# Optimization experiments

Hardware: AMD Instinct MI355X
Metric: run time of the kernel (lower is better)

## Reference

```python
import jax, jax.numpy as jnp
import numpy as np
import math

D_MODEL = 128
N_HEADS = 8
D_FF = 512
FACTOR = 3
EPS = 1e-5


def _ln(x, g, b):
    mu = x.mean(-1, keepdims=True)
    var = ((x - mu) ** 2).mean(-1, keepdims=True)
    return (x - mu) / jnp.sqrt(var + EPS) * g + b


def setup_inputs() -> dict:
    key = jax.random.key(0)
    ks = jax.random.split(key, 16)
    d, dff = D_MODEL, D_FF
    s = 0.02
    return {
        "x": jax.random.normal(ks[0], (4, 32, 256), dtype=jnp.float32),
        "mlp_w": jax.random.normal(ks[1], (d,)) * s,  # Conv2d(1,d,1x1) weight squeezed
        "mlp_b": jnp.zeros((d,), jnp.float32),
        "wq": jax.random.normal(ks[2], (d, d)) * s, "bq": jnp.zeros((d,), jnp.float32),
        "wk": jax.random.normal(ks[3], (d, d)) * s, "bk": jnp.zeros((d,), jnp.float32),
        "wv": jax.random.normal(ks[4], (d, d)) * s, "bv": jnp.zeros((d,), jnp.float32),
        "wo": jax.random.normal(ks[5], (d, d)) * s, "bo": jnp.zeros((d,), jnp.float32),
        "w1": jax.random.normal(ks[6], (dff, d)) * s, "b1": jnp.zeros((dff,), jnp.float32),
        "w2": jax.random.normal(ks[7], (d, dff)) * s, "b2": jnp.zeros((d,), jnp.float32),
        "ln1_g": jnp.ones((d,), jnp.float32), "ln1_b": jnp.zeros((d,), jnp.float32),
        "ln2_g": jnp.ones((d,), jnp.float32), "ln2_b": jnp.zeros((d,), jnp.float32),
    }


def reference(x, mlp_w, mlp_b, wq, bq, wk, bk, wv, bv, wo, bo,
              w1, b1, w2, b2, ln1_g, ln1_b, ln2_g, ln2_b):
    b, N, T = x.shape
    C, H = D_MODEL, N_HEADS
    E = C // H
    # 1x1 Conv2d from 1 channel -> per-channel affine of scalar input
    h = x[..., None] * mlp_w + mlp_b                      # [b,N,T,C]
    h = h.reshape(b * N, T, C)                            # [B,L,C]
    B, L = h.shape[0], T
    q = (h @ wq.T + bq).reshape(B, L, H, E).transpose(0, 2, 1, 3)  # [B,H,L,E]
    k = (h @ wk.T + bk).reshape(B, L, H, E).transpose(0, 2, 1, 3)
    v = (h @ wv.T + bv).reshape(B, L, H, E).transpose(0, 2, 1, 3)

    sample_k = min(FACTOR * math.ceil(math.log(L)), L)
    u = min(FACTOR * math.ceil(math.log(L)), L)
    # random K-sample indices shared across batch/heads (torch.randint analogue)
    idx = jax.random.randint(jax.random.key(42), (L, sample_k), 0, L)

    scores_full = jnp.einsum('bhle,bhse->bhls', q, k)     # [B,H,L,L]
    qk_sample = jnp.take_along_axis(scores_full, idx[None, None], axis=-1)  # [B,H,L,sample_k]
    M = qk_sample.max(-1) - qk_sample.sum(-1) / L         # sparsity measure
    m_top = jax.lax.top_k(M, u)[1]                        # [B,H,u] top-u query indices
    scores_top = jnp.take_along_axis(scores_full, m_top[..., None], axis=2)  # [B,H,u,L]
    scores_top = scores_top / math.sqrt(E)

    attn = jax.nn.softmax(scores_top, axis=-1)
    upd = jnp.einsum('bhul,bhle->bhue', attn, v)          # [B,H,u,E]
    # mask_flag=False: initial context = mean(V) broadcast over queries
    context = jnp.broadcast_to(v.mean(axis=2, keepdims=True), v.shape)
    bi = jnp.arange(B)[:, None, None]
    hi = jnp.arange(H)[None, :, None]
    context = context.at[bi, hi, m_top].set(upd)          # scatter top-u updates

    out = context.transpose(0, 2, 1, 3).reshape(B, L, C) @ wo.T + bo
    x1 = _ln(h + out, ln1_g, ln1_b)
    y = jax.nn.relu(x1 @ w1.T + b1) @ w2.T + b2           # 1x1 conv1d pair == MLP
    out2 = _ln(x1 + y, ln2_g, ln2_b)
    out2 = out2.reshape(b, N, T, C).sum(axis=1)           # sum over N
    return out2.transpose(0, 2, 1)                        # [b,C,T]
```

## Files before the change

kernel.cpp:

```cpp
#include <hip/hip_runtime.h>
#include <stdint.h>
#include <math.h>


#define EPSF 1e-5f

typedef short bf16x8 __attribute__((ext_vector_type(8)));
typedef float f32x4  __attribute__((ext_vector_type(4)));

__device__ __forceinline__ unsigned short f2bf(float f) {
  union { float f; unsigned u; } v; v.f = f;
  unsigned r = v.u + 0x7FFFu + ((v.u >> 16) & 1u);
  return (unsigned short)(r >> 16);
}
__device__ __forceinline__ float bf2f(unsigned short u) {
  union { unsigned u; float f; } v; v.u = ((unsigned)u) << 16;
  return v.f;
}
__device__ __forceinline__ float waveSum(float v) {
  #pragma unroll
  for (int m = 32; m > 0; m >>= 1) v += __shfl_xor(v, m);
  return v;
}

__device__ __forceinline__ void threefry2x32_k42(uint32_t& x0, uint32_t& x1) {
  const uint32_t ks0 = 0u, ks1 = 42u, ks2 = 0u ^ 42u ^ 0x1BD11BDAu;
  x0 += ks0; x1 += ks1;
#define TF_R(d) { x0 += x1; x1 = (x1 << d) | (x1 >> (32 - d)); x1 ^= x0; }
  TF_R(13) TF_R(15) TF_R(26) TF_R(6)  x0 += ks1; x1 += ks2 + 1u;
  TF_R(17) TF_R(29) TF_R(16) TF_R(24) x0 += ks2; x1 += ks0 + 2u;
  TF_R(13) TF_R(15) TF_R(26) TF_R(6)  x0 += ks0; x1 += ks1 + 3u;
  TF_R(17) TF_R(29) TF_R(16) TF_R(24) x0 += ks1; x1 += ks2 + 4u;
  TF_R(13) TF_R(15) TF_R(26) TF_R(6)  x0 += ks2; x1 += ks0 + 5u;
#undef TF_R
}

__global__ __launch_bounds__(256) void setup_kernel(
    const float* __restrict__ mlp_w, const float* __restrict__ mlp_b,
    const float* __restrict__ wq, const float* __restrict__ bq,
    const float* __restrict__ wk, const float* __restrict__ bk,
    const float* __restrict__ wv, const float* __restrict__ bv,
    const float* __restrict__ wo, const float* __restrict__ bo,
    const float* __restrict__ w1, const float* __restrict__ w2,
    int* __restrict__ idxT, float* __restrict__ cst,
    unsigned short* __restrict__ w1s, unsigned short* __restrict__ w2s) {
  int tid = threadIdx.x;
  {
    int fid = blockIdx.x * 256 + tid;
    const float* s;
    unsigned short* d;
    if (fid < 8192) {
      int lane = fid & 63; int tmp = fid >> 6;
      int ft = tmp & 3; tmp >>= 2;
      int ks = tmp & 3; tmp >>= 2;
      int ch = tmp & 1; int w = tmp >> 1;
      int col = lane & 15, quad = lane >> 4;
      int f = w * 128 + ch * 64 + ft * 16 + col;
      int k = ks * 32 + quad * 8;
      s = w1 + f * 128 + k;
      d = w1s + fid * 8;
    } else {
      int G = fid - 8192;
      int lane = G & 63; int tmp = G >> 6;
      int tc = tmp & 7; tmp >>= 3;
      int kk = tmp & 1; tmp >>= 1;
      int ch = tmp & 1; int w = tmp >> 1;
      int col = lane & 15, quad = lane >> 4;
      int c = tc * 16 + col;
      int k = w * 128 + ch * 64 + kk * 32 + quad * 8;
      s = w2 + c * 512 + k;
      d = w2s + G * 8;
    }
    float4 v0 = *(const float4*)s, v1 = *(const float4*)(s + 4);
    uint4 pk;
    pk.x = (unsigned)f2bf(v0.x) | ((unsigned)f2bf(v0.y) << 16);
    pk.y = (unsigned)f2bf(v0.z) | ((unsigned)f2bf(v0.w) << 16);
    pk.z = (unsigned)f2bf(v1.x) | ((unsigned)f2bf(v1.y) << 16);
    pk.w = (unsigned)f2bf(v1.z) | ((unsigned)f2bf(v1.w) << 16);
    *(uint4*)d = pk;
  }
  if (blockIdx.x != 0) return;
  for (int p = tid; p < 2304; p += 256) {
    uint32_t a = (uint32_t)p, bb = (uint32_t)(p + 2304);
    threefry2x32_k42(a, bb);
    int l0 = p / 18, j0 = p - l0 * 18;
    int p2 = p + 2304;
    int l1 = p2 / 18, j1 = p2 - l1 * 18;
    idxT[j0 * 256 + l0] = (int)(a & 0xFFu);
    idxT[j1 * 256 + l1] = (int)(bb & 0xFFu);
  }
  if (tid < 128) {
    float aq = 0.f, cq_ = 0.f, ak = 0.f, ck_ = 0.f, av = 0.f, cv_ = 0.f;
    for (int c = 0; c < 128; c++) {
      float w = mlp_w[c], bb = mlp_b[c];
      float q = wq[tid * 128 + c], k = wk[tid * 128 + c], v = wv[tid * 128 + c];
      aq += q * w; cq_ += q * bb;
      ak += k * w; ck_ += k * bb;
      av += v * w; cv_ += v * bb;
    }
    cst[0   + tid] = aq;
    cst[128 + tid] = cq_ + bq[tid];
    cst[256 + tid] = ak;
    cst[384 + tid] = ck_ + bk[tid];
    cst[512 + tid] = av;
    cst[640 + tid] = cv_ + bv[tid];
  }
  __syncthreads();
  if (tid < 8) {
    float a = 0.f, b = 0.f, g = 0.f, d = 0.f;
    for (int e = 0; e < 16; e++) {
      int j = tid * 16 + e;
      float Aq = cst[j], Cq = cst[128 + j], Ak = cst[256 + j], Ck = cst[384 + j];
      a += Aq * Ak; b += Aq * Ck; g += Cq * Ak; d += Cq * Ck;
    }
    cst[768 + tid] = a; cst[776 + tid] = b; cst[784 + tid] = g; cst[792 + tid] = d;
  }
  if (tid < 128) {
    float oc = 0.f;
    for (int h = 0; h < 8; h++) {
      float s = 0.f;
      for (int e = 0; e < 16; e++) {
        float w = wo[tid * 128 + h * 16 + e];
        s  += w * cst[512 + h * 16 + e];
        oc += w * cst[640 + h * 16 + e];
      }
      cst[800 + h * 128 + tid] = s;
    }
    cst[1824 + tid] = oc + bo[tid] + mlp_b[tid];
  }
}

__global__ __launch_bounds__(256) void attn_kernel(
    const float* __restrict__ x, const int* __restrict__ idxT,
    const float* __restrict__ cst, float* __restrict__ g) {
  __shared__ float xr[256];
  __shared__ float Mb[512];
  __shared__ float selv[512];
  __shared__ float rsum[4], rmax[4], rmin[4];
  __shared__ int   items[64];
  __shared__ float witem[64];
  __shared__ int   cnt;
  int tid = threadIdx.x, lane = tid & 63, w = tid >> 6;
  int seq = blockIdx.x >> 2, hg = blockIdx.x & 3;
  if (tid == 0) cnt = 0;
  float xv = x[seq * 256 + tid];
  xr[tid] = xv;
  float s = waveSum(xv);
  float mx = xv, mn = xv;
  #pragma unroll
  for (int m = 32; m > 0; m >>= 1) {
    mx = fmaxf(mx, __shfl_xor(mx, m));
    mn = fminf(mn, __shfl_xor(mn, m));
  }
  if (lane == 0) { rsum[w] = s; rmax[w] = mx; rmin[w] = mn; }
  __syncthreads();
  float meanx = (rsum[0] + rsum[1] + rsum[2] + rsum[3]) * (1.0f / 256.0f);
  float maxx = fmaxf(fmaxf(rmax[0], rmax[1]), fmaxf(rmax[2], rmax[3]));
  float minx = fminf(fminf(rmin[0], rmin[1]), fminf(rmin[2], rmin[3]));
  int l32 = tid & 31, grp = tid >> 5;
  float xs8[8];
  #pragma unroll
  for (int k = 0; k < 8; k++) xs8[k] = xr[l32 + k * 32];
  float mx18 = -INFINITY, mn18 = INFINITY, s18 = 0.f;
  #pragma unroll 3
  for (int j = 0; j < 18; j++) {
    float xs = xr[idxT[j * 256 + tid]];
    mx18 = fmaxf(mx18, xs); mn18 = fminf(mn18, xs); s18 += xs;
  }
  int h0 = hg * 2, h1 = h0 + 1;
  float al0 = cst[768 + h0], be0 = cst[776 + h0], ga0 = cst[784 + h0], de0 = cst[792 + h0];
  float al1 = cst[768 + h1], be1 = cst[776 + h1], ga1 = cst[784 + h1], de1 = cst[792 + h1];
  float ac0 = fmaf(al0, xv, ga0), cc0 = fmaf(be0, xv, de0);
  float ac1 = fmaf(al1, xv, ga1), cc1 = fmaf(be1, xv, de1);
  float M0 = ((ac0 >= 0.f ? ac0 * mx18 : ac0 * mn18) + cc0)
           - (fmaf(ac0, s18, 18.f * cc0)) * (1.0f / 256.0f);
  float M1 = ((ac1 >= 0.f ? ac1 * mx18 : ac1 * mn18) + cc1)
           - (fmaf(ac1, s18, 18.f * cc1)) * (1.0f / 256.0f);
  Mb[tid] = M0; Mb[256 + tid] = M1;
  __syncthreads();
  int r0 = 0, r1 = 0;
  const float4* Mb4 = (const float4*)Mb;
  #pragma unroll 4
  for (int j4 = 0; j4 < 64; j4++) {
    float4 a = Mb4[j4], bb = Mb4[64 + j4];
    int base = j4 * 4;
    r0 += (a.x > M0) || (a.x == M0 && base     < tid);
    r0 += (a.y > M0) || (a.y == M0 && base + 1 < tid);
    r0 += (a.z > M0) || (a.z == M0 && base + 2 < tid);
    r0 += (a.w > M0) || (a.w == M0 && base + 3 < tid);
    r1 += (bb.x > M1) || (bb.x == M1 && base     < tid);
    r1 += (bb.y > M1) || (bb.y == M1 && base + 1 < tid);
    r1 += (bb.z > M1) || (bb.z == M1 && base + 2 < tid);
    r1 += (bb.w > M1) || (bb.w == M1 && base + 3 < tid);
  }
  selv[tid] = meanx; selv[256 + tid] = meanx;
  if (r0 < 18) { int p = atomicAdd(&cnt, 1); items[p] = tid;       witem[p] = 0.25f * ac0; }
  if (r1 < 18) { int p = atomicAdd(&cnt, 1); items[p] = 256 + tid; witem[p] = 0.25f * ac1; }
  __syncthreads();
  int nIt = cnt;
  for (int i = grp; i < nIt; i += 8) {
    int it = items[i]; float wv = witem[i];
    float m0 = (wv >= 0.f) ? wv * maxx : wv * minx;
    float S1 = 0.f, Sx = 0.f;
    #pragma unroll
    for (int k = 0; k < 8; k++) {
      float e = __expf(fmaf(wv, xs8[k], -m0));
      S1 += e; Sx = fmaf(xs8[k], e, Sx);
    }
    #pragma unroll
    for (int m = 16; m > 0; m >>= 1) {
      S1 += __shfl_xor(S1, m); Sx += __shfl_xor(Sx, m);
    }
    if (l32 == 0) selv[it] = Sx / S1;
  }
  __syncthreads();
  float2 gv; gv.x = selv[tid]; gv.y = selv[256 + tid];
  *(float2*)&g[(size_t)((seq << 8) + tid) * 8 + hg * 2] = gv;
}

__global__ __launch_bounds__(256, 3) void mega_kernel(
    const float* __restrict__ x, const float* __restrict__ g,
    const float* __restrict__ cst, const float* __restrict__ mlp_w,
    const unsigned short* __restrict__ w1s, const float* __restrict__ b1,
    const unsigned short* __restrict__ w2s, const float* __restrict__ b2,
    const float* __restrict__ ln1g, const float* __restrict__ ln1b,
    const float* __restrict__ ln2g, const float* __restrict__ ln2b,
    float* __restrict__ out) {
  __shared__ unsigned short x1s[32 * 136];
  __shared__ unsigned short tbuf[4 * 2304];
  __shared__ float psum[512];
  int tid = threadIdx.x, lane = tid & 63, w = tid >> 6;
  int col = lane & 15, quad = lane >> 4;
  int b = blockIdx.x >> 8, t = blockIdx.x & 255;
  unsigned short* tb = tbuf + w * 2304;

  {
    int c0 = lane << 1;
    float mwa = mlp_w[c0], mwb = mlp_w[c0 | 1];
    float cca = cst[1824 + c0], ccb = cst[1824 + (c0 | 1)];
    float wva[8], wvb[8];
    #pragma unroll
    for (int h = 0; h < 8; h++) {
      wva[h] = cst[800 + h * 128 + c0];
      wvb[h] = cst[800 + h * 128 + (c0 | 1)];
    }
    float g1a = ln1g[c0], g1b = ln1g[c0 | 1];
    float e1a = ln1b[c0], e1b = ln1b[c0 | 1];
    #pragma unroll
    for (int bt = 0; bt < 2; bt++) {
      float xv4[4]; float4 gA[4], gB[4];
      #pragma unroll
      for (int k = 0; k < 4; k++) {
        int n = w * 8 + bt * 4 + k;
        int tok = ((b * 32 + n) << 8) + t;
        xv4[k] = x[tok];
        gA[k] = *(const float4*)(g + (size_t)tok * 8);
        gB[k] = *(const float4*)(g + (size_t)tok * 8 + 4);
      }
      float ra[4], rb[4], su[4];
      #pragma unroll
      for (int k = 0; k < 4; k++) {
        float a_ = fmaf(xv4[k], mwa, cca), b_ = fmaf(xv4[k], mwb, ccb);
        a_ = fmaf(gA[k].x, wva[0], a_); b_ = fmaf(gA[k].x, wvb[0], b_);
        a_ = fmaf(gA[k].y, wva[1], a_); b_ = fmaf(gA[k].y, wvb[1], b_);
        a_ = fmaf(gA[k].z, wva[2], a_); b_ = fmaf(gA[k].z, wvb[2], b_);
        a_ = fmaf(gA[k].w, wva[3], a_); b_ = fmaf(gA[k].w, wvb[3], b_);
        a_ = fmaf(gB[k].x, wva[4], a_); b_ = fmaf(gB[k].x, wvb[4], b_);
        a_ = fmaf(gB[k].y, wva[5], a_); b_ = fmaf(gB[k].y, wvb[5], b_);
        a_ = fmaf(gB[k].z, wva[6], a_); b_ = fmaf(gB[k].z, wvb[6], b_);
        a_ = fmaf(gB[k].w, wva[7], a_); b_ = fmaf(gB[k].w, wvb[7], b_);
        ra[k] = a_; rb[k] = b_; su[k] = a_ + b_;
      }
      #pragma unroll
      for (int m = 32; m > 0; m >>= 1) {
        su[0] += __shfl_xor(su[0], m); su[1] += __shfl_xor(su[1], m);
        su[2] += __shfl_xor(su[2], m); su[3] += __shfl_xor(su[3], m);
      }
      float vs[4], da[4], db[4];
      #pragma unroll
      for (int k = 0; k < 4; k++) {
        float mu = su[k] * (1.0f / 128.0f);
        da[k] = ra[k] - mu; db[k] = rb[k] - mu;
        vs[k] = da[k] * da[k] + db[k] * db[k];
      }
      #pragma unroll
      for (int m = 32; m > 0; m >>= 1) {
        vs[0] += __shfl_xor(vs[0], m); vs[1] += __shfl_xor(vs[1], m);
        vs[2] += __shfl_xor(vs[2], m); vs[3] += __shfl_xor(vs[3], m);
      }
      #pragma unroll
      for (int k = 0; k < 4; k++) {
        int n = w * 8 + bt * 4 + k;
        float inv = rsqrtf(vs[k] * (1.0f / 128.0f) + EPSF);
        unsigned int pa = f2bf(da[k] * inv * g1a + e1a);
        unsigned int pb = f2bf(db[k] * inv * g1b + e1b);
        *(unsigned int*)&x1s[n * 136 + c0] = pa | (pb << 16);
      }
    }
  }
  __syncthreads();

  float b1v[2][4];
  #pragma unroll
  for (int ch = 0; ch < 2; ch++)
    #pragma unroll
    for (int ft = 0; ft < 4; ft++)
      b1v[ch][ft] = b1[w * 128 + ch * 64 + ft * 16 + col];

  f32x4 acc2[2][8];
  #pragma unroll
  for (int i = 0; i < 2; i++)
    #pragma unroll
    for (int j = 0; j < 8; j++) acc2[i][j] = (f32x4){0.f, 0.f, 0.f, 0.f};

  #pragma unroll
  for (int ch = 0; ch < 2; ch++) {
    const unsigned short* w1p = w1s + (w * 2 + ch) * 8192 + lane * 8;
    const unsigned short* w2p = w2s + (w * 2 + ch) * 8192 + lane * 8;
    f32x4 acc1[2][4];
    #pragma unroll
    for (int i = 0; i < 2; i++)
      #pragma unroll
      for (int j = 0; j < 4; j++) acc1[i][j] = (f32x4){0.f, 0.f, 0.f, 0.f};
    #pragma unroll
    for (int ks = 0; ks < 4; ks++) {
      bf16x8 a0 = *(const bf16x8*)&x1s[col * 136 + ks * 32 + quad * 8];
      bf16x8 a1 = *(const bf16x8*)&x1s[(16 + col) * 136 + ks * 32 + quad * 8];
      #pragma unroll
      for (int ft = 0; ft < 4; ft++) {
        bf16x8 bw = *(const bf16x8*)(w1p + ks * 2048 + ft * 512);
        acc1[0][ft] = __builtin_amdgcn_mfma_f32_16x16x32_bf16(a0, bw, acc1[0][ft], 0, 0, 0);
        acc1[1][ft] = __builtin_amdgcn_mfma_f32_16x16x32_bf16(a1, bw, acc1[1][ft], 0, 0, 0);
      }
    }
    #pragma unroll
    for (int ft = 0; ft < 4; ft++) {
      #pragma unroll
      for (int rg = 0; rg < 2; rg++) {
        #pragma unroll
        for (int r = 0; r < 4; r++) {
          float vv = fmaxf(acc1[rg][ft][r] + b1v[ch][ft], 0.f);
          tb[(rg * 16 + quad * 4 + r) * 72 + ft * 16 + col] = f2bf(vv);
        }
      }
    }
    #pragma unroll
    for (int kk = 0; kk < 2; kk++) {
      bf16x8 a0 = *(const bf16x8*)&tb[col * 72 + kk * 32 + quad * 8];
      bf16x8 a1 = *(const bf16x8*)&tb[(16 + col) * 72 + kk * 32 + quad * 8];
      #pragma unroll
      for (int tc = 0; tc < 8; tc++) {
        bf16x8 bw = *(const bf16x8*)(w2p + kk * 4096 + tc * 512);
        acc2[0][tc] = __builtin_amdgcn_mfma_f32_16x16x32_bf16(a0, bw, acc2[0][tc], 0, 0, 0);
        acc2[1][tc] = __builtin_amdgcn_mfma_f32_16x16x32_bf16(a1, bw, acc2[1][tc], 0, 0, 0);
      }
    }
  }

  int row16 = tid >> 4, c8 = (tid & 15) << 3;
  float b2v[8], g2v[8], e2v[8];
  {
    float4 a0 = *(const float4*)(b2 + c8),  a1 = *(const float4*)(b2 + c8 + 4);
    float4 b0 = *(const float4*)(ln2g + c8), b1_ = *(const float4*)(ln2g + c8 + 4);
    float4 c0 = *(const float4*)(ln2b + c8), c1 = *(const float4*)(ln2b + c8 + 4);
    b2v[0]=a0.x; b2v[1]=a0.y; b2v[2]=a0.z; b2v[3]=a0.w;
    b2v[4]=a1.x; b2v[5]=a1.y; b2v[6]=a1.z; b2v[7]=a1.w;
    g2v[0]=b0.x; g2v[1]=b0.y; g2v[2]=b0.z; g2v[3]=b0.w;
    g2v[4]=b1_.x; g2v[5]=b1_.y; g2v[6]=b1_.z; g2v[7]=b1_.w;
    e2v[0]=c0.x; e2v[1]=c0.y; e2v[2]=c0.z; e2v[3]=c0.w;
    e2v[4]=c1.x; e2v[5]=c1.y; e2v[6]=c1.z; e2v[7]=c1.w;
  }
  float res[2][8];
  #pragma unroll
  for (int p = 0; p < 2; p++) {
    bf16x8 rv = *(const bf16x8*)&x1s[(p * 16 + row16) * 136 + c8];
    #pragma unroll
    for (int k = 0; k < 8; k++) res[p][k] = bf2f((unsigned short)rv[k]);
  }

  #pragma unroll
  for (int p = 0; p < 2; p++) {
    if (p) __syncthreads();
    #pragma unroll
    for (int tc = 0; tc < 8; tc++) {
      #pragma unroll
      for (int r = 0; r < 4; r++)
        tb[(quad * 4 + r) * 136 + tc * 16 + col] = f2bf(acc2[p][tc][r]);
    }
    __syncthreads();
    float z[8];
    #pragma unroll
    for (int k = 0; k < 8; k++) z[k] = b2v[k] + res[p][k];
    #pragma unroll
    for (int ws = 0; ws < 4; ws++) {
      bf16x8 v = *(const bf16x8*)&tbuf[ws * 2304 + row16 * 136 + c8];
      #pragma unroll
      for (int k = 0; k < 8; k++) z[k] += bf2f((unsigned short)v[k]);
    }
    float s = 0.f;
    #pragma unroll
    for (int k = 0; k < 8; k++) s += z[k];
    #pragma unroll
    for (int m = 1; m <= 8; m <<= 1) s += __shfl_xor(s, m);
    float mu = s * (1.0f / 128.0f);
    float q = 0.f;
    #pragma unroll
    for (int k = 0; k < 8; k++) { float d = z[k] - mu; q += d * d; }
    #pragma unroll
    for (int m = 1; m <= 8; m <<= 1) q += __shfl_xor(q, m);
    float inv = rsqrtf(q * (1.0f / 128.0f) + EPSF);
    float o[8];
    #pragma unroll
    for (int k = 0; k < 8; k++) o[k] = (z[k] - mu) * inv * g2v[k] + e2v[k];
    #pragma unroll
    for (int k = 0; k < 8; k++) {
      o[k] += __shfl_xor(o[k], 16);
      o[k] += __shfl_xor(o[k], 32);
    }
    if (lane < 16) {
      float* pp = &psum[w * 128 + lane * 8];
      if (p == 0) {
        #pragma unroll
        for (int k = 0; k < 8; k++) pp[k] = o[k];
      } else {
        #pragma unroll
        for (int k = 0; k < 8; k++) pp[k] += o[k];
      }
    }
  }
  __syncthreads();
  if (tid < 128) {
    float v = psum[tid] + psum[128 + tid] + psum[256 + tid] + psum[384 + tid];
    out[(size_t)(b * 128 + tid) * 256 + t] = v;
  }
}

extern "C" void kernel_launch(void* const* d_in, const int* in_sizes, int n_in,
                              void* d_out, int out_size, void* d_ws, size_t ws_size,
                              hipStream_t stream) {
  (void)in_sizes; (void)n_in; (void)out_size; (void)ws_size;
  const float* x    = (const float*)d_in[0];
  const float* mlpw = (const float*)d_in[1];
  const float* mlpb = (const float*)d_in[2];
  const float* wq   = (const float*)d_in[3];
  const float* bq   = (const float*)d_in[4];
  const float* wk   = (const float*)d_in[5];
  const float* bk   = (const float*)d_in[6];
  const float* wv   = (const float*)d_in[7];
  const float* bv   = (const float*)d_in[8];
  const float* wo   = (const float*)d_in[9];
  const float* bo   = (const float*)d_in[10];
  const float* w1   = (const float*)d_in[11];
  const float* b1   = (const float*)d_in[12];
  const float* w2   = (const float*)d_in[13];
  const float* b2   = (const float*)d_in[14];
  const float* ln1g = (const float*)d_in[15];
  const float* ln1b = (const float*)d_in[16];
  const float* ln2g = (const float*)d_in[17];
  const float* ln2b = (const float*)d_in[18];

  char* ws = (char*)d_ws;
  int*            idxT = (int*)(ws);
  float*          cst  = (float*)(ws + 20480);
  unsigned short* w1s  = (unsigned short*)(ws + 32768);
  unsigned short* w2s  = (unsigned short*)(ws + 163840);
  float*          gbuf = (float*)(ws + 294912);
  float*          outp = (float*)d_out;

  hipLaunchKernelGGL(setup_kernel, dim3(64), dim3(256), 0, stream,
                     mlpw, mlpb, wq, bq, wk, bk, wv, bv, wo, bo, w1, w2,
                     idxT, cst, w1s, w2s);
  hipLaunchKernelGGL(attn_kernel, dim3(512), dim3(256), 0, stream,
                     x, idxT, cst, gbuf);
  hipLaunchKernelGGL(mega_kernel, dim3(1024), dim3(256), 0, stream,
                     x, gbuf, cst, mlpw, w1s, b1, w2s, b2,
                     ln1g, ln1b, ln2g, ln2b, outp);
}
```

Before: 151.1 us.

## Software-pipeline FFN chunks and raise mega_kernel occupancy bound

Unrolls the two FFN hidden chunks by hand so the second chunk's W1 MFMAs are issued before the first chunk's W2 MFMAs, hoists the x1 fragments from LDS into registers once, and raises the launch-bounds minimum blocks from 3 to 4. It also adds an unconditional barrier before the output staging so tb reuse is safe. The aim is to overlap matrix work with LDS round-trips and raise occupancy. The cost is more live registers (acc1b, xa0/xa1), which may spill under the tighter 4-block register cap.

```diff
diff --git a/kernel.cpp b/kernel.cpp
--- a/kernel.cpp
+++ b/kernel.cpp
@@ -218,7 +218,7 @@
   *(float2*)&g[(size_t)((seq << 8) + tid) * 8 + hg * 2] = gv;
 }
 
-__global__ __launch_bounds__(256, 3) void mega_kernel(
+__global__ __launch_bounds__(256, 4) void mega_kernel(
     const float* __restrict__ x, const float* __restrict__ g,
     const float* __restrict__ cst, const float* __restrict__ mlp_w,
     const unsigned short* __restrict__ w1s, const float* __restrict__ b1,
@@ -307,53 +307,91 @@
     for (int ft = 0; ft < 4; ft++)
       b1v[ch][ft] = b1[w * 128 + ch * 64 + ft * 16 + col];
 
+  const unsigned short* w1p0 = w1s + (w * 2 + 0) * 8192 + lane * 8;
+  const unsigned short* w1p1 = w1s + (w * 2 + 1) * 8192 + lane * 8;
+  const unsigned short* w2p0 = w2s + (w * 2 + 0) * 8192 + lane * 8;
+  const unsigned short* w2p1 = w2s + (w * 2 + 1) * 8192 + lane * 8;
+
   f32x4 acc2[2][8];
   #pragma unroll
   for (int i = 0; i < 2; i++)
     #pragma unroll
     for (int j = 0; j < 8; j++) acc2[i][j] = (f32x4){0.f, 0.f, 0.f, 0.f};
 
-  #pragma unroll
-  for (int ch = 0; ch < 2; ch++) {
-    const unsigned short* w1p = w1s + (w * 2 + ch) * 8192 + lane * 8;
-    const unsigned short* w2p = w2s + (w * 2 + ch) * 8192 + lane * 8;
-    f32x4 acc1[2][4];
-    #pragma unroll
-    for (int i = 0; i < 2; i++)
-      #pragma unroll
-      for (int j = 0; j < 4; j++) acc1[i][j] = (f32x4){0.f, 0.f, 0.f, 0.f};
-    #pragma unroll
-    for (int ks = 0; ks < 4; ks++) {
-      bf16x8 a0 = *(const bf16x8*)&x1s[col * 136 + ks * 32 + quad * 8];
-      bf16x8 a1 = *(const bf16x8*)&x1s[(16 + col) * 136 + ks * 32 + quad * 8];
-      #pragma unroll
-      for (int ft = 0; ft < 4; ft++) {
-        bf16x8 bw = *(const bf16x8*)(w1p + ks * 2048 + ft * 512);
-        acc1[0][ft] = __builtin_amdgcn_mfma_f32_16x16x32_bf16(a0, bw, acc1[0][ft], 0, 0, 0);
-        acc1[1][ft] = __builtin_amdgcn_mfma_f32_16x16x32_bf16(a1, bw, acc1[1][ft], 0, 0, 0);
-      }
-    }
+  bf16x8 xa0[4], xa1[4];
+  #pragma unroll
+  for (int ks = 0; ks < 4; ks++) {
+    xa0[ks] = *(const bf16x8*)&x1s[col * 136 + ks * 32 + quad * 8];
+    xa1[ks] = *(const bf16x8*)&x1s[(16 + col) * 136 + ks * 32 + quad * 8];
+  }
+
+  f32x4 acc1[2][4];
+
+  #pragma unroll
+  for (int i = 0; i < 2; i++)
+    #pragma unroll
+    for (int j = 0; j < 4; j++) acc1[i][j] = (f32x4){0.f, 0.f, 0.f, 0.f};
+  #pragma unroll
+  for (int ks = 0; ks < 4; ks++) {
     #pragma unroll
     for (int ft = 0; ft < 4; ft++) {
-      #pragma unroll
-      for (int rg = 0; rg < 2; rg++) {
-        #pragma unroll
-        for (int r = 0; r < 4; r++) {
-          float vv = fmaxf(acc1[rg][ft][r] + b1v[ch][ft], 0.f);
-          tb[(rg * 16 + quad * 4 + r) * 72 + ft * 16 + col] = f2bf(vv);
-        }
-      }
-    }
-    #pragma unroll
-    for (int kk = 0; kk < 2; kk++) {
-      bf16x8 a0 = *(const bf16x8*)&tb[col * 72 + kk * 32 + quad * 8];
-      bf16x8 a1 = *(const bf16x8*)&tb[(16 + col) * 72 + kk * 32 + quad * 8];
-      #pragma unroll
-      for (int tc = 0; tc < 8; tc++) {
-        bf16x8 bw = *(const bf16x8*)(w2p + kk * 4096 + tc * 512);
-        acc2[0][tc] = __builtin_amdgcn_mfma_f32_16x16x32_bf16(a0, bw, acc2[0][tc], 0, 0, 0);
-        acc2[1][tc] = __builtin_amdgcn_mfma_f32_16x16x32_bf16(a1, bw, acc2[1][tc], 0, 0, 0);
-      }
+      bf16x8 bw = *(const bf16x8*)(w1p0 + ks * 2048 + ft * 512);
+      acc1[0][ft] = __builtin_amdgcn_mfma_f32_16x16x32_bf16(xa0[ks], bw, acc1[0][ft], 0, 0, 0);
+      acc1[1][ft] = __builtin_amdgcn_mfma_f32_16x16x32_bf16(xa1[ks], bw, acc1[1][ft], 0, 0, 0);
+    }
+  }
+  #pragma unroll
+  for (int ft = 0; ft < 4; ft++)
+    #pragma unroll
+    for (int rg = 0; rg < 2; rg++)
+      #pragma unroll
+      for (int r = 0; r < 4; r++) {
+        float vv = fmaxf(acc1[rg][ft][r] + b1v[0][ft], 0.f);
+        tb[(rg * 16 + quad * 4 + r) * 72 + ft * 16 + col] = f2bf(vv);
+      }
+  f32x4 acc1b[2][4];
+  #pragma unroll
+  for (int i = 0; i < 2; i++)
+    #pragma unroll
+    for (int j = 0; j < 4; j++) acc1b[i][j] = (f32x4){0.f, 0.f, 0.f, 0.f};
+  #pragma unroll
+  for (int ks = 0; ks < 4; ks++) {
+    #pragma unroll
+    for (int ft = 0; ft < 4; ft++) {
+      bf16x8 bw = *(const bf16x8*)(w1p1 + ks * 2048 + ft * 512);
+      acc1b[0][ft] = __builtin_amdgcn_mfma_f32_16x16x32_bf16(xa0[ks], bw, acc1b[0][ft], 0, 0, 0);
+      acc1b[1][ft] = __builtin_amdgcn_mfma_f32_16x16x32_bf16(xa1[ks], bw, acc1b[1][ft], 0, 0, 0);
+    }
+  }
+  #pragma unroll
+  for (int kk = 0; kk < 2; kk++) {
+    bf16x8 a0 = *(const bf16x8*)&tb[col * 72 + kk * 32 + quad * 8];
+    bf16x8 a1 = *(const bf16x8*)&tb[(16 + col) * 72 + kk * 32 + quad * 8];
+    #pragma unroll
+    for (int tc = 0; tc < 8; tc++) {
+      bf16x8 bw = *(const bf16x8*)(w2p0 + kk * 4096 + tc * 512);
+      acc2[0][tc] = __builtin_amdgcn_mfma_f32_16x16x32_bf16(a0, bw, acc2[0][tc], 0, 0, 0);
+      acc2[1][tc] = __builtin_amdgcn_mfma_f32_16x16x32_bf16(a1, bw, acc2[1][tc], 0, 0, 0);
+    }
+  }
+  #pragma unroll
+  for (int ft = 0; ft < 4; ft++)
+    #pragma unroll
+    for (int rg = 0; rg < 2; rg++)
+      #pragma unroll
+      for (int r = 0; r < 4; r++) {
+        float vv = fmaxf(acc1b[rg][ft][r] + b1v[1][ft], 0.f);
+        tb[(rg * 16 + quad * 4 + r) * 72 + ft * 16 + col] = f2bf(vv);
+      }
+  #pragma unroll
+  for (int kk = 0; kk < 2; kk++) {
+    bf16x8 a0 = *(const bf16x8*)&tb[col * 72 + kk * 32 + quad * 8];
+    bf16x8 a1 = *(const bf16x8*)&tb[(16 + col) * 72 + kk * 32 + quad * 8];
+    #pragma unroll
+    for (int tc = 0; tc < 8; tc++) {
+      bf16x8 bw = *(const bf16x8*)(w2p1 + kk * 4096 + tc * 512);
+      acc2[0][tc] = __builtin_amdgcn_mfma_f32_16x16x32_bf16(a0, bw, acc2[0][tc], 0, 0, 0);
+      acc2[1][tc] = __builtin_amdgcn_mfma_f32_16x16x32_bf16(a1, bw, acc2[1][tc], 0, 0, 0);
     }
   }
 
@@ -380,7 +418,7 @@
 
   #pragma unroll
   for (int p = 0; p < 2; p++) {
-    if (p) __syncthreads();
+    __syncthreads();
     #pragma unroll
     for (int tc = 0; tc < 8; tc++) {
       #pragma unroll
```

Result: no change. 152.9 us (+1.2%).
